# Optimization experiments

Hardware: AMD Instinct MI355X
Metric: run time of the kernel (lower is better)

Reference implementation:

```python
import jax, jax.numpy as jnp
import numpy as np

B, C, CE, DK, DV, H, W = 2, 64, 96, 64, 64, 96, 96
EPS = 1e-6


def setup_inputs() -> dict:
    key = jax.random.key(0)
    ks = jax.random.split(key, 8)
    s = lambda fan_in: 1.0 / np.sqrt(fan_in)
    return {
        "x": jax.random.normal(ks[0], (B, C, H, W), jnp.float32),
        "x_enc": jax.random.normal(ks[1], (B, CE, H, W), jnp.float32),
        "Wq": jax.random.uniform(ks[2], (DK, CE), jnp.float32, -s(CE), s(CE)),
        "bq": jax.random.uniform(ks[3], (DK,), jnp.float32, -s(CE), s(CE)),
        "Wk": jax.random.uniform(ks[4], (DK, CE), jnp.float32, -s(CE), s(CE)),
        "bk": jax.random.uniform(ks[5], (DK,), jnp.float32, -s(CE), s(CE)),
        "Wv": jax.random.uniform(ks[6], (DV, C), jnp.float32, -s(C), s(C)),
        "bv": jax.random.uniform(ks[7], (DV,), jnp.float32, -s(C), s(C)),
    }


def _l2norm(t):
    # F.normalize(dim=1): divide by channel-dim L2 norm, clamped at eps
    n = jnp.maximum(jnp.linalg.norm(t, axis=1, keepdims=True), EPS)
    return t / n


def reference(x, x_enc, Wq, bq, Wk, bk, Wv, bv):
    # 1x1 conv projections == pointwise channel GEMMs
    Q = jnp.einsum('oc,bchw->bohw', Wq, x_enc) + bq[None, :, None, None]
    K = jnp.einsum('oc,bchw->bohw', Wk, x_enc) + bk[None, :, None, None]
    V = jnp.einsum('oc,bchw->bohw', Wv, x) + bv[None, :, None, None]
    vshape = V.shape
    Q = _l2norm(Q.reshape(B, DK, H * W))  # [B, dk, L]
    K = _l2norm(K.reshape(B, DK, H * W))
    V = V.reshape(B, DV, H * W)           # [B, dv, L]
    # cosine-similarity attention over all spatial positions: A is [B, L, L]
    A = jax.nn.softmax(jnp.einsum('bqi,bqj->bij', Q, K), axis=-1)
    R = jnp.einsum('bij,bvj->bvi', A, V)   # [B, dv, L]
    return R.reshape(vshape)
```

## Files before the change

### kernel.cpp

```cpp
#include <hip/hip_runtime.h>

#define L_ 9216

typedef unsigned int uint;
typedef unsigned short ushort;
typedef __attribute__((ext_vector_type(8))) short short8;
typedef __attribute__((ext_vector_type(4))) float f32x4;
typedef __attribute__((ext_vector_type(16))) float f32x16;
typedef __attribute__((ext_vector_type(4))) unsigned uint4v;
typedef __attribute__((ext_vector_type(2))) unsigned uint2v;

#define MFMA32(a, b, c) __builtin_amdgcn_mfma_f32_32x32x16_bf16(a, b, c, 0, 0, 0)

#if __has_builtin(__builtin_amdgcn_exp2f)
#define EXP2(x) __builtin_amdgcn_exp2f(x)
#else
#define EXP2(x) exp2f(x)
#endif

#define GLOAD_LDS16(g, l)                                            \
  __builtin_amdgcn_global_load_lds(                                  \
      (const __attribute__((address_space(1))) unsigned int*)(g),    \
      (__attribute__((address_space(3))) unsigned int*)(l), 16, 0, 0)

union B8 {
  uint4v u;
  short8 s;
};

__device__ __forceinline__ ushort f2bf(float f) {
  uint u = __float_as_uint(f);
  return (ushort)((u + 0x7fffu + ((u >> 16) & 1u)) >> 16);
}

__device__ __forceinline__ f32x16 zero16() {
  f32x16 v;
#pragma unroll
  for (int i = 0; i < 16; i++) v[i] = 0.f;
  return v;
}

__global__ __launch_bounds__(256) void prep_kernel(
    const float* __restrict__ Wq, const float* __restrict__ Wk,
    const float* __restrict__ Wv, ushort* __restrict__ Wqb,
    ushort* __restrict__ Wkb, ushort* __restrict__ Wvb) {
  int i = blockIdx.x * 256 + threadIdx.x;
  if (i < 6144) {
    Wqb[i] = f2bf(Wq[i]);
    Wkb[i] = f2bf(Wk[i]);
  }
  if (i < 4096) Wvb[i] = f2bf(Wv[i]);
}

template <int CC, int TASK>
__device__ __forceinline__ void projm_body(
    const float* __restrict__ X,
    const ushort* __restrict__ Wb,
    const float* __restrict__ bias,
    ushort* __restrict__ dst) {
  constexpr int NKT = CC / 16;
  const int bx = blockIdx.x;
  const int b = bx / 288;
  const int p0 = (bx - b * 288) * 32;
  const int lane = threadIdx.x;
  const int ql = lane & 31;
  const int hs = lane >> 5;

  const float* Xb = X + (size_t)b * CC * L_ + p0 + ql;
  float xv[NKT * 8];
#pragma unroll
  for (int kt = 0; kt < NKT; kt++)
#pragma unroll
    for (int i = 0; i < 8; i++)
      xv[kt * 8 + i] = Xb[(size_t)(kt * 16 + hs * 8 + i) * L_];

  B8 bfr[NKT];
#pragma unroll
  for (int kt = 0; kt < NKT; kt++)
#pragma unroll
    for (int j = 0; j < 4; j++) {
      uint lo = f2bf(xv[kt * 8 + 2 * j]);
      uint hi = f2bf(xv[kt * 8 + 2 * j + 1]);
      bfr[kt].u[j] = lo | (hi << 16);
    }

  const ushort* Wr0 = Wb + (size_t)ql * CC + hs * 8;
  const ushort* Wr1 = Wb + (size_t)(32 + ql) * CC + hs * 8;

  f32x16 a0 = zero16(), a1 = zero16();
#pragma unroll
  for (int kt = 0; kt < NKT; kt++) {
    short8 w0 = *(const short8*)(Wr0 + kt * 16);
    short8 w1 = *(const short8*)(Wr1 + kt * 16);
    a0 = MFMA32(w0, bfr[kt].s, a0);
    a1 = MFMA32(w1, bfr[kt].s, a1);
  }

#pragma unroll
  for (int g = 0; g < 4; g++) {
    float4 b0 = *(const float4*)(bias + 8 * g + 4 * hs);
    float4 b1 = *(const float4*)(bias + 32 + 8 * g + 4 * hs);
    a0[4 * g + 0] += b0.x; a0[4 * g + 1] += b0.y;
    a0[4 * g + 2] += b0.z; a0[4 * g + 3] += b0.w;
    a1[4 * g + 0] += b1.x; a1[4 * g + 1] += b1.y;
    a1[4 * g + 2] += b1.z; a1[4 * g + 3] += b1.w;
  }

  if (TASK < 2) {
    float ss = 0.f;
#pragma unroll
    for (int r = 0; r < 16; r++) ss += a0[r] * a0[r] + a1[r] * a1[r];
    ss += __shfl_xor(ss, 32);
    float i0 = 1.0f / fmaxf(sqrtf(ss), 1e-6f);
    if (TASK == 0) i0 *= 1.44269504f;
    uint* d = (uint*)(dst + ((size_t)(b * L_ + p0 + ql)) * 64);
#pragma unroll
    for (int g = 0; g < 4; g++) {
      uint2v u0, u1;
      u0[0] = (uint)f2bf(a0[4 * g + 0] * i0) | ((uint)f2bf(a0[4 * g + 1] * i0) << 16);
      u0[1] = (uint)f2bf(a0[4 * g + 2] * i0) | ((uint)f2bf(a0[4 * g + 3] * i0) << 16);
      u1[0] = (uint)f2bf(a1[4 * g + 0] * i0) | ((uint)f2bf(a1[4 * g + 1] * i0) << 16);
      u1[1] = (uint)f2bf(a1[4 * g + 2] * i0) | ((uint)f2bf(a1[4 * g + 3] * i0) << 16);
      *(uint2v*)(d + 4 * g + 2 * hs) = u0;
      *(uint2v*)(d + 16 + 4 * g + 2 * hs) = u1;
    }
  } else {
#pragma unroll
    for (int r = 0; r < 16; r++) {
      int dv0 = (r & 3) + 8 * (r >> 2) + 4 * hs;
      dst[(size_t)(b * 64 + dv0) * L_ + p0 + ql] = f2bf(a0[r]);
      dst[(size_t)(b * 64 + 32 + dv0) * L_ + p0 + ql] = f2bf(a1[r]);
    }
  }
}

__global__ __launch_bounds__(64) void projm_kernel(
    const float* __restrict__ x, const float* __restrict__ x_enc,
    const ushort* __restrict__ Wqb, const float* __restrict__ bq,
    const ushort* __restrict__ Wkb, const float* __restrict__ bk,
    const ushort* __restrict__ Wvb, const float* __restrict__ bv,
    ushort* __restrict__ Qb, ushort* __restrict__ Kb,
    ushort* __restrict__ Vb) {
  const int task = blockIdx.y;
  if (task == 0)
    projm_body<96, 0>(x_enc, Wqb, bq, Qb);
  else if (task == 1)
    projm_body<96, 1>(x_enc, Wkb, bk, Kb);
  else
    projm_body<64, 2>(x, Wvb, bv, Vb);
}

__global__ __launch_bounds__(512, 4) void attn_kernel(
    const ushort* __restrict__ Qb, const ushort* __restrict__ Kb,
    const ushort* __restrict__ Vb, ushort* __restrict__ OP,
    float* __restrict__ LB, int tps) {
  __shared__ __align__(16) ushort KV_l[3][2][4096];

  const int nwg = gridDim.x;
  const int chunk = nwg >> 3;
  const int bid = blockIdx.x;
  const int logical = (bid & 7) * chunk + (bid >> 3);
  const int split = logical / 72;
  const int qidx = logical - split * 72;
  const int b = qidx / 36;
  const int q0 = (qidx - b * 36) * 256;

  const int t = threadIdx.x;
  const int lane = t & 63;
  const int w = t >> 6;
  const int ql = lane & 31;
  const int hs = lane >> 5;

  const ushort* Kg = Kb + (size_t)b * L_ * 64;
  const ushort* Vg = Vb + (size_t)b * 64 * L_;

  const int qrow = q0 + w * 32 + ql;
  const ushort* Qr = Qb + ((size_t)(b * L_ + qrow)) * 64 + hs * 8;
  short8 qf[4];
  qf[0] = *(const short8*)(Qr);
  qf[1] = *(const short8*)(Qr + 16);
  qf[2] = *(const short8*)(Qr + 32);
  qf[3] = *(const short8*)(Qr + 48);

  B8 onesu;
  onesu.u[0] = 0x3F803F80u;
  onesu.u[1] = 0x3F803F80u;
  onesu.u[2] = 0x3F803F80u;
  onesu.u[3] = 0x3F803F80u;

  f32x16 o[2];
  o[0] = zero16();
  o[1] = zero16();
  f32x16 od = zero16();

  const int ksw = (ql & 7) << 3;
  const char* lds0 = (const char*)&KV_l[0][0][0];
  int arf[4];
#pragma unroll
  for (int m = 0; m < 4; m++)
    arf[m] = (ql * 64 + ((m * 16 + hs * 8) ^ ksw)) * 2;

  const int rr = t >> 3, pl = t & 7;
  const int psrc = (pl ^ (rr & 7)) << 3;
  const int j0base = split * tps * 64;

#define STAGE(buf, j0)                                                     \
  {                                                                        \
    GLOAD_LDS16(Kg + (size_t)(j0)*64 + rr * 64 + psrc,                     \
                &KV_l[buf][0][w * 512]);                                   \
    GLOAD_LDS16(Vg + (size_t)rr * L_ + (j0) + psrc,                        \
                &KV_l[buf][1][w * 512]);                                   \
  }

  STAGE(0, j0base);
  STAGE(1, j0base + 64);

  for (int t3 = 0; t3 < tps; t3 += 3) {
#pragma unroll
    for (int ib = 0; ib < 3; ib++) {
      const int tt = t3 + ib;
      if (tt + 1 < tps) {
        asm volatile("s_waitcnt vmcnt(2)" ::: "memory");
      } else {
        asm volatile("s_waitcnt vmcnt(0)" ::: "memory");
      }
      __builtin_amdgcn_s_barrier();
      __builtin_amdgcn_sched_barrier(0);
      if (tt + 2 < tps) {
        STAGE((ib + 2) % 3, j0base + (tt + 2) * 64);
      }

      B8 pf[4];
#pragma unroll
      for (int st = 0; st < 2; st++) {
        f32x16 sa = zero16();
        __builtin_amdgcn_s_setprio(1);
#pragma unroll
        for (int m = 0; m < 4; m++) {
          short8 kf = *(const short8*)(lds0 + arf[m] + ib * 16384 + st * 4096);
          sa = MFMA32(kf, qf[m], sa);
        }
        __builtin_amdgcn_s_setprio(0);
        uint Wp[8];
#pragma unroll
        for (int c = 0; c < 4; c++)
#pragma unroll
          for (int rp = 0; rp < 2; rp++) {
            int i0 = 4 * c + 2 * rp;
            float p0 = EXP2(sa[i0]);
            float p1 = EXP2(sa[i0 + 1]);
            Wp[2 * c + rp] = __builtin_amdgcn_perm(
                __float_as_uint(p1), __float_as_uint(p0), 0x07060302u);
          }
#pragma unroll
        for (int u = 0; u < 2; u++) {
          auto ra = __builtin_amdgcn_permlane32_swap(Wp[4 * u + 0],
                                                     Wp[4 * u + 2], false,
                                                     false);
          auto rb = __builtin_amdgcn_permlane32_swap(Wp[4 * u + 1],
                                                     Wp[4 * u + 3], false,
                                                     false);
          uint4v fw;
          fw[0] = ra[0];
          fw[1] = rb[0];
          fw[2] = ra[1];
          fw[3] = rb[1];
          pf[st * 2 + u].u = fw;
        }
      }

      __builtin_amdgcn_s_setprio(1);
#pragma unroll
      for (int s = 0; s < 4; s++) od = MFMA32(onesu.s, pf[s].s, od);

#pragma unroll
      for (int dt = 0; dt < 2; dt++) {
#pragma unroll
        for (int s = 0; s < 4; s++) {
          short8 vf = *(const short8*)(lds0 + arf[s] + ib * 16384 + 8192 +
                                       dt * 4096);
          o[dt] = MFMA32(vf, pf[s].s, o[dt]);
        }
      }
      __builtin_amdgcn_s_setprio(0);
    }
  }

  if (hs == 0) LB[(size_t)split * 2 * L_ + (size_t)b * L_ + qrow] = od[0];

  ushort* Ob = OP + (size_t)split * 2 * 64 * L_;
#pragma unroll
  for (int dt = 0; dt < 2; dt++)
#pragma unroll
    for (int r = 0; r < 16; r++) {
      int dv = dt * 32 + (r & 3) + 8 * (r >> 2) + 4 * hs;
      Ob[(size_t)(b * 64 + dv) * L_ + qrow] = f2bf(o[dt][r]);
    }
}

template <int NS>
__global__ __launch_bounds__(256) void combine_kernel(
    const ushort* __restrict__ OP, const float* __restrict__ LB,
    float* __restrict__ out) {
  const size_t e = ((size_t)blockIdx.x * 256 + threadIdx.x) * 8;
  const int bdv = (int)(e / L_);
  const int b = bdv >> 6;
  const int q = (int)(e % L_);
  float os[8], ls[8];
#pragma unroll
  for (int i = 0; i < 8; i++) { os[i] = 0.f; ls[i] = 0.f; }
#pragma unroll
  for (int s = 0; s < NS; s++) {
    uint4v pv = *(const uint4v*)(OP + (size_t)s * 2 * 64 * L_ + e);
    const float* lp = LB + (size_t)s * 2 * L_ + (size_t)b * L_ + q;
    f32x4 l0 = *(const f32x4*)(lp);
    f32x4 l1 = *(const f32x4*)(lp + 4);
#pragma unroll
    for (int i = 0; i < 4; i++) {
      os[2 * i] += __uint_as_float(pv[i] << 16);
      os[2 * i + 1] += __uint_as_float(pv[i] & 0xFFFF0000u);
      ls[i] += l0[i];
      ls[4 + i] += l1[i];
    }
  }
  float r[8];
#pragma unroll
  for (int i = 0; i < 8; i++) r[i] = os[i] / ls[i];
  *(f32x4*)(out + e) = *(const f32x4*)&r[0];
  *(f32x4*)(out + e + 4) = *(const f32x4*)&r[4];
}

extern "C" void kernel_launch(void* const* d_in, const int* in_sizes, int n_in,
                              void* d_out, int out_size, void* d_ws, size_t ws_size,
                              hipStream_t stream) {
  const float* x = (const float*)d_in[0];
  const float* x_enc = (const float*)d_in[1];
  const float* Wq = (const float*)d_in[2];
  const float* bq = (const float*)d_in[3];
  const float* Wk = (const float*)d_in[4];
  const float* bk = (const float*)d_in[5];
  const float* Wv = (const float*)d_in[6];
  const float* bv = (const float*)d_in[7];
  float* out = (float*)d_out;

  ushort* Qb = (ushort*)d_ws;
  ushort* Kb = Qb + (size_t)2 * L_ * 64;
  ushort* Vb = Kb + (size_t)2 * L_ * 64;
  ushort* Wqb = Vb + (size_t)2 * L_ * 64;
  ushort* Wkb = Wqb + 6144;
  ushort* Wvb = Wkb + 6144;
  const size_t qkv_bytes = (size_t)3 * 2 * L_ * 64 * 2 + 2 * (6144 + 6144 + 4096);
  const size_t per_split = (size_t)2 * 64 * L_ * 2 + (size_t)2 * L_ * 4;

  int SPLIT = 16;
  while (SPLIT > 1 && qkv_bytes + (size_t)SPLIT * per_split > ws_size) SPLIT >>= 1;

  ushort* OP = (ushort*)((char*)d_ws + qkv_bytes);
  float* LB = (float*)(OP + (size_t)SPLIT * 2 * 64 * L_);

  prep_kernel<<<24, 256, 0, stream>>>(Wq, Wk, Wv, Wqb, Wkb, Wvb);
  projm_kernel<<<dim3(576, 3), 64, 0, stream>>>(x, x_enc, Wqb, bq, Wkb, bk,
                                                Wvb, bv, Qb, Kb, Vb);
  attn_kernel<<<72 * SPLIT, 512, 0, stream>>>(Qb, Kb, Vb, OP, LB, 144 / SPLIT);
  const int cgrid = (2 * 64 * L_ / 8) / 256;
  if (SPLIT == 16)
    combine_kernel<16><<<cgrid, 256, 0, stream>>>(OP, LB, out);
  else if (SPLIT == 8)
    combine_kernel<8><<<cgrid, 256, 0, stream>>>(OP, LB, out);
  else if (SPLIT == 4)
    combine_kernel<4><<<cgrid, 256, 0, stream>>>(OP, LB, out);
  else if (SPLIT == 2)
    combine_kernel<2><<<cgrid, 256, 0, stream>>>(OP, LB, out);
  else
    combine_kernel<1><<<cgrid, 256, 0, stream>>>(OP, LB, out);
}
```

Before: 82.92 us.

## Software-pipeline QK^T of next tile with PV of current tile using 4-stage LDS ring

Restructures the attention loop so the QK^T MFMAs and exp/pack for tile t+1 are issued alongside the PV and denominator MFMAs for tile t, with double-buffered P fragments. The LDS ring grows from three to four stages so loads run three tiles ahead. The split count and tiles-per-split become compile-time constants (16 and 9), and the occupancy hint of 4 waves per SIMD is dropped from launch bounds. Register pressure and LDS use both rise, which can cut occupancy. The workspace-size fallback is removed, so the code assumes enough scratch space exists.

```diff
diff --git a/kernel.cpp b/kernel.cpp
--- a/kernel.cpp
+++ b/kernel.cpp
@@ -1,6 +1,7 @@
 #include <hip/hip_runtime.h>
 
 #define L_ 9216
+#define TPS 9
 
 typedef unsigned int uint;
 typedef unsigned short ushort;
@@ -150,11 +151,11 @@
     projm_body<64, 2>(x, Wvb, bv, Vb);
 }
 
-__global__ __launch_bounds__(512, 4) void attn_kernel(
+__global__ __launch_bounds__(512) void attn_kernel(
     const ushort* __restrict__ Qb, const ushort* __restrict__ Kb,
     const ushort* __restrict__ Vb, ushort* __restrict__ OP,
-    float* __restrict__ LB, int tps) {
-  __shared__ __align__(16) ushort KV_l[3][2][4096];
+    float* __restrict__ LB) {
+  __shared__ __align__(16) ushort KV_l[4][2][4096];
 
   const int nwg = gridDim.x;
   const int chunk = nwg >> 3;
@@ -202,7 +203,7 @@
 
   const int rr = t >> 3, pl = t & 7;
   const int psrc = (pl ^ (rr & 7)) << 3;
-  const int j0base = split * tps * 64;
+  const int j0base = split * TPS * 64;
 
 #define STAGE(buf, j0)                                                     \
   {                                                                        \
@@ -212,79 +213,101 @@
                 &KV_l[buf][1][w * 512]);                                   \
   }
 
+#define QKMM(BUF, s0, s1)                                                  \
+  {                                                                        \
+    __builtin_amdgcn_s_setprio(1);                                         \
+    _Pragma("unroll") for (int m = 0; m < 4; m++) {                        \
+      short8 kf0 = *(const short8*)(lds0 + arf[m] + (BUF)*16384);          \
+      short8 kf1 = *(const short8*)(lds0 + arf[m] + (BUF)*16384 + 4096);   \
+      s0 = MFMA32(kf0, qf[m], s0);                                         \
+      s1 = MFMA32(kf1, qf[m], s1);                                         \
+    }                                                                      \
+    __builtin_amdgcn_s_setprio(0);                                         \
+  }
+
+#define SMPK1(sa, pf, st)                                                  \
+  {                                                                        \
+    uint Wp[8];                                                            \
+    _Pragma("unroll") for (int c = 0; c < 4; c++) _Pragma("unroll")        \
+        for (int rp = 0; rp < 2; rp++) {                                   \
+      int i0 = 4 * c + 2 * rp;                                             \
+      float p0 = EXP2(sa[i0]);                                             \
+      float p1 = EXP2(sa[i0 + 1]);                                         \
+      Wp[2 * c + rp] = __builtin_amdgcn_perm(__float_as_uint(p1),          \
+                                             __float_as_uint(p0),          \
+                                             0x07060302u);                 \
+    }                                                                      \
+    _Pragma("unroll") for (int u = 0; u < 2; u++) {                        \
+      auto ra = __builtin_amdgcn_permlane32_swap(Wp[4 * u + 0],            \
+                                                 Wp[4 * u + 2], false,     \
+                                                 false);                   \
+      auto rb = __builtin_amdgcn_permlane32_swap(Wp[4 * u + 1],            \
+                                                 Wp[4 * u + 3], false,     \
+                                                 false);                   \
+      uint4v fw;                                                           \
+      fw[0] = ra[0];                                                       \
+      fw[1] = rb[0];                                                       \
+      fw[2] = ra[1];                                                       \
+      fw[3] = rb[1];                                                       \
+      pf[(st)*2 + u].u = fw;                                               \
+    }                                                                      \
+  }
+
+#define PVDEN(BUF, pf)                                                     \
+  {                                                                        \
+    __builtin_amdgcn_s_setprio(1);                                         \
+    _Pragma("unroll") for (int s = 0; s < 4; s++) od =                     \
+        MFMA32(onesu.s, pf[s].s, od);                                      \
+    _Pragma("unroll") for (int dt = 0; dt < 2; dt++) {                     \
+      _Pragma("unroll") for (int s = 0; s < 4; s++) {                      \
+        short8 vf = *(const short8*)(lds0 + arf[s] + (BUF)*16384 + 8192 +  \
+                                     dt * 4096);                           \
+        o[dt] = MFMA32(vf, pf[s].s, o[dt]);                                \
+      }                                                                    \
+    }                                                                      \
+    __builtin_amdgcn_s_setprio(0);                                         \
+  }
+
+  B8 pfA[4], pfB[4];
+
   STAGE(0, j0base);
   STAGE(1, j0base + 64);
-
-  for (int t3 = 0; t3 < tps; t3 += 3) {
-#pragma unroll
-    for (int ib = 0; ib < 3; ib++) {
-      const int tt = t3 + ib;
-      if (tt + 1 < tps) {
-        asm volatile("s_waitcnt vmcnt(2)" ::: "memory");
-      } else {
-        asm volatile("s_waitcnt vmcnt(0)" ::: "memory");
-      }
-      __builtin_amdgcn_s_barrier();
-      __builtin_amdgcn_sched_barrier(0);
-      if (tt + 2 < tps) {
-        STAGE((ib + 2) % 3, j0base + (tt + 2) * 64);
-      }
-
-      B8 pf[4];
-#pragma unroll
-      for (int st = 0; st < 2; st++) {
-        f32x16 sa = zero16();
-        __builtin_amdgcn_s_setprio(1);
-#pragma unroll
-        for (int m = 0; m < 4; m++) {
-          short8 kf = *(const short8*)(lds0 + arf[m] + ib * 16384 + st * 4096);
-          sa = MFMA32(kf, qf[m], sa);
-        }
-        __builtin_amdgcn_s_setprio(0);
-        uint Wp[8];
-#pragma unroll
-        for (int c = 0; c < 4; c++)
-#pragma unroll
-          for (int rp = 0; rp < 2; rp++) {
-            int i0 = 4 * c + 2 * rp;
-            float p0 = EXP2(sa[i0]);
-            float p1 = EXP2(sa[i0 + 1]);
-            Wp[2 * c + rp] = __builtin_amdgcn_perm(
-                __float_as_uint(p1), __float_as_uint(p0), 0x07060302u);
-          }
-#pragma unroll
-        for (int u = 0; u < 2; u++) {
-          auto ra = __builtin_amdgcn_permlane32_swap(Wp[4 * u + 0],
-                                                     Wp[4 * u + 2], false,
-                                                     false);
-          auto rb = __builtin_amdgcn_permlane32_swap(Wp[4 * u + 1],
-                                                     Wp[4 * u + 3], false,
-                                                     false);
-          uint4v fw;
-          fw[0] = ra[0];
-          fw[1] = rb[0];
-          fw[2] = ra[1];
-          fw[3] = rb[1];
-          pf[st * 2 + u].u = fw;
-        }
-      }
-
-      __builtin_amdgcn_s_setprio(1);
-#pragma unroll
-      for (int s = 0; s < 4; s++) od = MFMA32(onesu.s, pf[s].s, od);
-
-#pragma unroll
-      for (int dt = 0; dt < 2; dt++) {
-#pragma unroll
-        for (int s = 0; s < 4; s++) {
-          short8 vf = *(const short8*)(lds0 + arf[s] + ib * 16384 + 8192 +
-                                       dt * 4096);
-          o[dt] = MFMA32(vf, pf[s].s, o[dt]);
-        }
-      }
-      __builtin_amdgcn_s_setprio(0);
-    }
-  }
+  STAGE(2, j0base + 128);
+  asm volatile("s_waitcnt vmcnt(4)" ::: "memory");
+  __builtin_amdgcn_s_barrier();
+  {
+    f32x16 s0 = zero16(), s1 = zero16();
+    QKMM(0, s0, s1);
+    SMPK1(s0, pfA, 0);
+    SMPK1(s1, pfA, 1);
+  }
+
+#define PIPE_ITER(ib, pfCUR, pfNXT)                                        \
+  {                                                                        \
+    const int tt = t4 + (ib);                                              \
+    if (tt + 2 < TPS) {                                                    \
+      asm volatile("s_waitcnt vmcnt(2)" ::: "memory");                     \
+    } else {                                                               \
+      asm volatile("s_waitcnt vmcnt(0)" ::: "memory");                     \
+    }                                                                      \
+    __builtin_amdgcn_s_barrier();                                          \
+    __builtin_amdgcn_sched_barrier(0);                                     \
+    if (tt + 3 < TPS) STAGE(((ib) + 3) & 3, j0base + (tt + 3) * 64);       \
+    f32x16 s0 = zero16(), s1 = zero16();                                   \
+    QKMM((((ib) + 1) & 3), s0, s1);                                        \
+    PVDEN(((ib)&3), pfCUR);                                                \
+    SMPK1(s0, pfNXT, 0);                                                   \
+    SMPK1(s1, pfNXT, 1);                                                   \
+  }
+
+  for (int t4 = 0; t4 < TPS - 1; t4 += 4) {
+    PIPE_ITER(0, pfA, pfB)
+    PIPE_ITER(1, pfB, pfA)
+    PIPE_ITER(2, pfA, pfB)
+    PIPE_ITER(3, pfB, pfA)
+  }
+
+  PVDEN(0, pfA);
 
   if (hs == 0) LB[(size_t)split * 2 * L_ + (size_t)b * L_ + qrow] = od[0];
 
@@ -350,27 +373,15 @@
   ushort* Wkb = Wqb + 6144;
   ushort* Wvb = Wkb + 6144;
   const size_t qkv_bytes = (size_t)3 * 2 * L_ * 64 * 2 + 2 * (6144 + 6144 + 4096);
-  const size_t per_split = (size_t)2 * 64 * L_ * 2 + (size_t)2 * L_ * 4;
-
-  int SPLIT = 16;
-  while (SPLIT > 1 && qkv_bytes + (size_t)SPLIT * per_split > ws_size) SPLIT >>= 1;
-
+
+  const int SPLIT = 16;
   ushort* OP = (ushort*)((char*)d_ws + qkv_bytes);
   float* LB = (float*)(OP + (size_t)SPLIT * 2 * 64 * L_);
 
   prep_kernel<<<24, 256, 0, stream>>>(Wq, Wk, Wv, Wqb, Wkb, Wvb);
   projm_kernel<<<dim3(576, 3), 64, 0, stream>>>(x, x_enc, Wqb, bq, Wkb, bk,
                                                 Wvb, bv, Qb, Kb, Vb);
-  attn_kernel<<<72 * SPLIT, 512, 0, stream>>>(Qb, Kb, Vb, OP, LB, 144 / SPLIT);
+  attn_kernel<<<72 * SPLIT, 512, 0, stream>>>(Qb, Kb, Vb, OP, LB);
   const int cgrid = (2 * 64 * L_ / 8) / 256;
-  if (SPLIT == 16)
-    combine_kernel<16><<<cgrid, 256, 0, stream>>>(OP, LB, out);
-  else if (SPLIT == 8)
-    combine_kernel<8><<<cgrid, 256, 0, stream>>>(OP, LB, out);
-  else if (SPLIT == 4)
-    combine_kernel<4><<<cgrid, 256, 0, stream>>>(OP, LB, out);
-  else if (SPLIT == 2)
-    combine_kernel<2><<<cgrid, 256, 0, stream>>>(OP, LB, out);
-  else
-    combine_kernel<1><<<cgrid, 256, 0, stream>>>(OP, LB, out);
-}
+  combine_kernel<16><<<cgrid, 256, 0, stream>>>(OP, LB, out);
+}
```

Result: slower. 86.91 us (+4.8%).
